# Kernel optimization log

Hardware: AMD Instinct MI355X
Metric: run time of the kernel (lower is better)

## Reference

```python
import jax, jax.numpy as jnp
import numpy as np

ALPHA = 0.2
NEG_BIG = -9e15

def setup_inputs() -> dict:
    key = jax.random.key(0)
    k1, k2, k3, k4 = jax.random.split(key, 4)
    B, N, F = 8, 2048, 256
    h = jax.random.normal(k1, (B, N, F), dtype=jnp.float32)
    adj = jax.random.randint(k2, (B, N, N), 0, 2, dtype=jnp.int32)
    W = jax.random.normal(k3, (F, F), dtype=jnp.float32) * (1.414 / jnp.sqrt(F))
    a = jax.random.normal(k4, (2 * F, 1), dtype=jnp.float32) * 0.1
    return {"h": h, "adj": adj, "W": W, "a": a}

def reference(h, adj, W, a):
    F_out = W.shape[1]
    Wh = jnp.einsum('bnf,fo->bno', h, W)            # [B,N,F]
    Wh1 = Wh @ a[:F_out]                             # [B,N,1]
    Wh2 = Wh @ a[F_out:]                             # [B,N,1]
    e = jax.nn.leaky_relu(Wh1 + jnp.swapaxes(Wh2, 1, 2), negative_slope=ALPHA)  # [B,N,N]
    scores = jnp.where(adj > 0, e, NEG_BIG)
    attention = jax.nn.softmax(scores, axis=-1)      # [B,N,N]
    h_prime = jnp.einsum('bnm,bmf->bnf', attention, Wh)
    out = h + jax.nn.elu(h_prime)                    # concat=True -> elu; residual add
    return (out, attention)
```

## Files before the change

kernel.cpp:

```cpp
#include <hip/hip_runtime.h>

#define NB 8
#define NN 2048
#define NF 256

typedef __attribute__((ext_vector_type(8))) short bf16x8;
typedef __attribute__((ext_vector_type(4))) float f32x4;
typedef __attribute__((ext_vector_type(4))) int i32x4;

__device__ __forceinline__ unsigned short f2bf(float x) {
  union { float f; unsigned int i; } c; c.f = x;
  unsigned int r = c.i + 0x7FFFu + ((c.i >> 16) & 1u);
  return (unsigned short)(r >> 16);
}
__device__ __forceinline__ unsigned short f2bf_fast(float x) {
  union { float f; unsigned int i; } c; c.f = x;
  return (unsigned short)((c.i + 0x8000u) >> 16);
}
__device__ __forceinline__ bf16x8 cvt8(float4 c0, float4 c1) {
  union { bf16x8 v8; unsigned short us[8]; } cu;
  cu.us[0] = f2bf_fast(c0.x); cu.us[1] = f2bf_fast(c0.y);
  cu.us[2] = f2bf_fast(c0.z); cu.us[3] = f2bf_fast(c0.w);
  cu.us[4] = f2bf_fast(c1.x); cu.us[5] = f2bf_fast(c1.y);
  cu.us[6] = f2bf_fast(c1.z); cu.us[7] = f2bf_fast(c1.w);
  return cu.v8;
}
__device__ __forceinline__ bf16x8 cvt8v(f32x4 c0, f32x4 c1) {
  union { bf16x8 v8; unsigned short us[8]; } cu;
  cu.us[0] = f2bf_fast(c0.x); cu.us[1] = f2bf_fast(c0.y);
  cu.us[2] = f2bf_fast(c0.z); cu.us[3] = f2bf_fast(c0.w);
  cu.us[4] = f2bf_fast(c1.x); cu.us[5] = f2bf_fast(c1.y);
  cu.us[6] = f2bf_fast(c1.z); cu.us[7] = f2bf_fast(c1.w);
  return cu.v8;
}

__global__ __launch_bounds__(256) void k_prep(
    const float* __restrict__ W, const float* __restrict__ a,
    unsigned short* __restrict__ WT, float* __restrict__ u, float* __restrict__ v) {
  int t = threadIdx.x;
  if (blockIdx.x < 256) {
    int k = blockIdx.x;
    WT[t * 256 + k] = f2bf(W[k * 256 + t]);
  } else {
    float su = 0.f, sv = 0.f;
    for (int o = 0; o < 256; ++o) {
      float w = W[t * 256 + o];
      su += w * a[o];
      sv += w * a[256 + o];
    }
    u[t] = su; v[t] = sv;
  }
}

__global__ __launch_bounds__(256) void k_mid(
    const float* __restrict__ h, const unsigned short* __restrict__ WTr,
    const float* __restrict__ u, const float* __restrict__ v,
    unsigned short* __restrict__ WhT, float* __restrict__ Wh1, float* __restrict__ Wh2) {
  int bx = blockIdx.x;
  int b = bx >> 7;
  int iW = (bx & 127) * 16;
  int wave = threadIdx.x >> 6, lane = threadIdx.x & 63;
  int fW = wave * 64;
  int l15 = lane & 15, q8 = (lane >> 4) * 8;
  const float* hB = h + (size_t)b * NN * NF;

  f32x4 acc[4];
#pragma unroll
  for (int ft = 0; ft < 4; ++ft) acc[ft] = (f32x4){0.f, 0.f, 0.f, 0.f};
  float su = 0.f, sv = 0.f;

  for (int k0 = 0; k0 < NF; k0 += 32) {
    int kk = k0 + q8;
    const float* p = hB + (size_t)(iW + l15) * NF + kk;
    float4 h0 = *(const float4*)p;
    float4 h1 = *(const float4*)(p + 4);
    bf16x8 bfr = cvt8(h0, h1);
    if (wave == 0) {
      const float* up = u + kk;
      const float* vp = v + kk;
      su += h0.x*up[0] + h0.y*up[1] + h0.z*up[2] + h0.w*up[3]
          + h1.x*up[4] + h1.y*up[5] + h1.z*up[6] + h1.w*up[7];
      sv += h0.x*vp[0] + h0.y*vp[1] + h0.z*vp[2] + h0.w*vp[3]
          + h1.x*vp[4] + h1.y*vp[5] + h1.z*vp[6] + h1.w*vp[7];
    }
#pragma unroll
    for (int ft = 0; ft < 4; ++ft) {
      bf16x8 af = *(const bf16x8*)(WTr + (fW + ft * 16 + l15) * 256 + kk);
      acc[ft] = __builtin_amdgcn_mfma_f32_16x16x32_bf16(af, bfr, acc[ft], 0, 0, 0);
    }
  }

  unsigned short* WhTb = WhT + (size_t)b * NF * NN;
  int q4 = (lane >> 4) * 4;
#pragma unroll
  for (int ft = 0; ft < 4; ++ft)
#pragma unroll
    for (int r = 0; r < 4; ++r) {
      int f = fW + ft * 16 + q4 + r;
      WhTb[(size_t)f * NN + iW + l15] = f2bf(acc[ft][r]);
    }

  if (wave == 0) {
    su += __shfl_xor(su, 16); su += __shfl_xor(su, 32);
    sv += __shfl_xor(sv, 16); sv += __shfl_xor(sv, 32);
    if (lane < 16) {
      Wh1[b * NN + iW + lane] = su;
      Wh2[b * NN + iW + lane] = sv;
    }
  }
}

__global__ __launch_bounds__(512, 4) void k_fuse(
    const int* __restrict__ adj, const float* __restrict__ Wh1,
    const float* __restrict__ Wh2, const unsigned short* __restrict__ WhT,
    const float* __restrict__ h, float* __restrict__ att, float* __restrict__ out) {
  __shared__ unsigned short satt[16 * 2048];
  const float NEGBIG = -9.0e15f;
  int bx = blockIdx.x;
  bx = (bx & 7) * 128 + (bx >> 3);
  int b = bx >> 7;
  int i0 = (bx & 127) * 16;
  int wave = threadIdx.x >> 6, lane = threadIdx.x & 63;
  const float* w2 = Wh2 + ((size_t)b << 11);

  int rowbase = b * NN + i0 + wave * 2;
#pragma unroll
  for (int rr = 0; rr < 2; ++rr) {
    const int* arow = adj + (size_t)(rowbase + rr) * NN;
    float w1 = Wh1[rowbase + rr];
    float x[32];
#pragma unroll
    for (int c = 0; c < 8; ++c) {
      int j = c * 256 + lane * 4;
      i32x4 av = __builtin_nontemporal_load((const i32x4*)(arow + j));
      float4 pv = *(const float4*)(w2 + j);
      float t;
      t = w1 + pv.x; t = t >= 0.f ? t : 0.2f * t; x[c*4+0] = (av.x > 0) ? t : NEGBIG;
      t = w1 + pv.y; t = t >= 0.f ? t : 0.2f * t; x[c*4+1] = (av.y > 0) ? t : NEGBIG;
      t = w1 + pv.z; t = t >= 0.f ? t : 0.2f * t; x[c*4+2] = (av.z > 0) ? t : NEGBIG;
      t = w1 + pv.w; t = t >= 0.f ? t : 0.2f * t; x[c*4+3] = (av.w > 0) ? t : NEGBIG;
    }

    float m = x[0];
#pragma unroll
    for (int k = 1; k < 32; ++k) m = fmaxf(m, x[k]);
#pragma unroll
    for (int off = 32; off >= 1; off >>= 1) m = fmaxf(m, __shfl_xor(m, off));
    float sum = 0.f;
#pragma unroll
    for (int k = 0; k < 32; ++k) { x[k] = __expf(x[k] - m); sum += x[k]; }
#pragma unroll
    for (int off = 32; off >= 1; off >>= 1) sum += __shfl_xor(sum, off);
    float iv = 1.0f / sum;

    int row_local = wave * 2 + rr;
    int swz = row_local * 8;
    float* orow = att + (size_t)(rowbase + rr) * NN;
    unsigned short* srow = satt + row_local * 2048;
#pragma unroll
    for (int c = 0; c < 8; ++c) {
      int j = c * 256 + lane * 4;
      float a0 = x[c*4+0] * iv, a1 = x[c*4+1] * iv;
      float a2 = x[c*4+2] * iv, a3 = x[c*4+3] * iv;
      f32x4 ov = (f32x4){a0, a1, a2, a3};
      __builtin_nontemporal_store(ov, (f32x4*)(orow + j));
      int e = ((j & ~7) ^ swz) + (j & 7);
      union { short4 v4; unsigned short us[4]; } pk;
      pk.us[0] = f2bf_fast(a0); pk.us[1] = f2bf_fast(a1);
      pk.us[2] = f2bf_fast(a2); pk.us[3] = f2bf_fast(a3);
      *(short4*)(srow + e) = pk.v4;
    }
  }

  __syncthreads();

  int fW = wave * 32;
  int l15 = lane & 15, q8 = (lane >> 4) * 8;
  const unsigned short* WTb = WhT + (size_t)b * NF * NN;
  const unsigned short* aRow = satt + l15 * 2048;
  int swzA = l15 * 8;

  f32x4 acc[2];
#pragma unroll
  for (int nt = 0; nt < 2; ++nt) acc[nt] = (f32x4){0.f, 0.f, 0.f, 0.f};

  for (int kk = 0; kk < NN; kk += 32) {
    bf16x8 afr = *(const bf16x8*)(aRow + (((kk + q8) ^ swzA)));
    bf16x8 bfr[2];
#pragma unroll
    for (int nt = 0; nt < 2; ++nt) {
      int f = fW + nt * 16 + l15;
      bfr[nt] = *(const bf16x8*)(WTb + (size_t)f * NN + kk + q8);
    }
#pragma unroll
    for (int nt = 0; nt < 2; ++nt)
      acc[nt] = __builtin_amdgcn_mfma_f32_16x16x32_bf16(afr, bfr[nt], acc[nt], 0, 0, 0);
  }

  int q4 = (lane >> 4) * 4;
#pragma unroll
  for (int nt = 0; nt < 2; ++nt)
#pragma unroll
    for (int r = 0; r < 4; ++r) {
      int i = i0 + q4 + r;
      int f = fW + nt * 16 + l15;
      size_t idx = ((size_t)(b * NN + i)) * NF + f;
      float hp = acc[nt][r];
      float el = hp > 0.f ? hp : expm1f(hp);
      float hv = __builtin_nontemporal_load(h + idx);
      __builtin_nontemporal_store(hv + el, out + idx);
    }
}

extern "C" void kernel_launch(void* const* d_in, const int* in_sizes, int n_in,
                              void* d_out, int out_size, void* d_ws, size_t ws_size,
                              hipStream_t stream) {
  const float* h = nullptr; const int* adj = nullptr;
  const float* W = nullptr; const float* a = nullptr;
  for (int i = 0; i < n_in; ++i) {
    int s = in_sizes[i];
    if (s == NB * NN * NF) h = (const float*)d_in[i];
    else if (s == NB * NN * NN) adj = (const int*)d_in[i];
    else if (s == NF * NF) W = (const float*)d_in[i];
    else if (s == 2 * NF) a = (const float*)d_in[i];
  }

  float* out = (float*)d_out;
  float* att = out + (size_t)NB * NN * NF;

  char* ws = (char*)d_ws;
  unsigned short* WhT = (unsigned short*)ws;
  unsigned short* WTr = (unsigned short*)(ws + 8388608);
  float* u   = (float*)(ws + 8388608 + 131072);
  float* v   = u + 256;
  float* Wh1 = v + 256;
  float* Wh2 = Wh1 + NB * NN;

  k_prep<<<257, 256, 0, stream>>>(W, a, WTr, u, v);
  k_mid<<<1024, 256, 0, stream>>>(h, WTr, u, v, WhT, Wh1, Wh2);
  k_fuse<<<NB * 128, 512, 0, stream>>>(adj, Wh1, Wh2, WhT, h, att, out);
}
```

Before: 406.7 us.

## Store WT and WhT in k-blocked tiles for contiguous MFMA operand loads

```diff
diff --git a/kernel.cpp b/kernel.cpp
--- a/kernel.cpp
+++ b/kernel.cpp
@@ -7,6 +7,7 @@
 typedef __attribute__((ext_vector_type(8))) short bf16x8;
 typedef __attribute__((ext_vector_type(4))) float f32x4;
 typedef __attribute__((ext_vector_type(4))) int i32x4;
+
 
 __device__ __forceinline__ unsigned short f2bf(float x) {
   union { float f; unsigned int i; } c; c.f = x;
@@ -25,14 +26,6 @@
   cu.us[6] = f2bf_fast(c1.z); cu.us[7] = f2bf_fast(c1.w);
   return cu.v8;
 }
-__device__ __forceinline__ bf16x8 cvt8v(f32x4 c0, f32x4 c1) {
-  union { bf16x8 v8; unsigned short us[8]; } cu;
-  cu.us[0] = f2bf_fast(c0.x); cu.us[1] = f2bf_fast(c0.y);
-  cu.us[2] = f2bf_fast(c0.z); cu.us[3] = f2bf_fast(c0.w);
-  cu.us[4] = f2bf_fast(c1.x); cu.us[5] = f2bf_fast(c1.y);
-  cu.us[6] = f2bf_fast(c1.z); cu.us[7] = f2bf_fast(c1.w);
-  return cu.v8;
-}
 
 __global__ __launch_bounds__(256) void k_prep(
     const float* __restrict__ W, const float* __restrict__ a,
@@ -40,7 +33,7 @@
   int t = threadIdx.x;
   if (blockIdx.x < 256) {
     int k = blockIdx.x;
-    WT[t * 256 + k] = f2bf(W[k * 256 + t]);
+    WT[(k >> 5) * 8192 + t * 32 + ((k >> 3) & 3) * 8 + (k & 7)] = f2bf(W[k * 256 + t]);
   } else {
     float su = 0.f, sv = 0.f;
     for (int o = 0; o < 256; ++o) {
@@ -61,13 +54,15 @@
   int iW = (bx & 127) * 16;
   int wave = threadIdx.x >> 6, lane = threadIdx.x & 63;
   int fW = wave * 64;
-  int l15 = lane & 15, q8 = (lane >> 4) * 8;
+  int l15 = lane & 15, gq = lane >> 4, q8 = gq * 8;
   const float* hB = h + (size_t)b * NN * NF;
 
   f32x4 acc[4];
 #pragma unroll
   for (int ft = 0; ft < 4; ++ft) acc[ft] = (f32x4){0.f, 0.f, 0.f, 0.f};
   float su = 0.f, sv = 0.f;
+
+  const unsigned short* wf = WTr + (fW + l15) * 32 + gq * 8;
 
   for (int k0 = 0; k0 < NF; k0 += 32) {
     int kk = k0 + q8;
@@ -83,21 +78,25 @@
       sv += h0.x*vp[0] + h0.y*vp[1] + h0.z*vp[2] + h0.w*vp[3]
           + h1.x*vp[4] + h1.y*vp[5] + h1.z*vp[6] + h1.w*vp[7];
     }
+    const unsigned short* wk = wf + (k0 >> 5) * 8192;
 #pragma unroll
     for (int ft = 0; ft < 4; ++ft) {
-      bf16x8 af = *(const bf16x8*)(WTr + (fW + ft * 16 + l15) * 256 + kk);
+      bf16x8 af = *(const bf16x8*)(wk + ft * 512);
       acc[ft] = __builtin_amdgcn_mfma_f32_16x16x32_bf16(af, bfr, acc[ft], 0, 0, 0);
     }
   }
 
   unsigned short* WhTb = WhT + (size_t)b * NF * NN;
-  int q4 = (lane >> 4) * 4;
+  int kb = iW >> 5;
+  int gg = ((iW & 16) + l15) >> 3;
+  int jj = l15 & 7;
+  int q4 = gq * 4;
 #pragma unroll
   for (int ft = 0; ft < 4; ++ft)
 #pragma unroll
     for (int r = 0; r < 4; ++r) {
       int f = fW + ft * 16 + q4 + r;
-      WhTb[(size_t)f * NN + iW + l15] = f2bf(acc[ft][r]);
+      WhTb[kb * 8192 + f * 32 + gg * 8 + jj] = f2bf(acc[ft][r]);
     }
 
   if (wave == 0) {
@@ -175,10 +174,11 @@
   __syncthreads();
 
   int fW = wave * 32;
-  int l15 = lane & 15, q8 = (lane >> 4) * 8;
+  int l15 = lane & 15, gq = lane >> 4, q8 = gq * 8;
   const unsigned short* WTb = WhT + (size_t)b * NF * NN;
   const unsigned short* aRow = satt + l15 * 2048;
   int swzA = l15 * 8;
+  const unsigned short* bbase = WTb + (fW + l15) * 32 + gq * 8;
 
   f32x4 acc[2];
 #pragma unroll
@@ -186,18 +186,14 @@
 
   for (int kk = 0; kk < NN; kk += 32) {
     bf16x8 afr = *(const bf16x8*)(aRow + (((kk + q8) ^ swzA)));
-    bf16x8 bfr[2];
-#pragma unroll
-    for (int nt = 0; nt < 2; ++nt) {
-      int f = fW + nt * 16 + l15;
-      bfr[nt] = *(const bf16x8*)(WTb + (size_t)f * NN + kk + q8);
-    }
-#pragma unroll
-    for (int nt = 0; nt < 2; ++nt)
-      acc[nt] = __builtin_amdgcn_mfma_f32_16x16x32_bf16(afr, bfr[nt], acc[nt], 0, 0, 0);
-  }
-
-  int q4 = (lane >> 4) * 4;
+    const unsigned short* bk = bbase + (kk >> 5) * 8192;
+    bf16x8 bfr0 = *(const bf16x8*)(bk);
+    bf16x8 bfr1 = *(const bf16x8*)(bk + 512);
+    acc[0] = __builtin_amdgcn_mfma_f32_16x16x32_bf16(afr, bfr0, acc[0], 0, 0, 0);
+    acc[1] = __builtin_amdgcn_mfma_f32_16x16x32_bf16(afr, bfr1, acc[1], 0, 0, 0);
+  }
+
+  int q4 = gq * 4;
 #pragma unroll
   for (int nt = 0; nt < 2; ++nt)
 #pragma unroll
```

Result: faster. 347.3 us (-14.6%).
